# Kernel tuning notes

Measured on AMD Instinct MI355X. Metric: run time of the kernel, lower is better.

Reference implementation:

```python
import jax, jax.numpy as jnp
import numpy as np

CHANNELS = 768
N_HEADS = 12
HEAD_DIM = CHANNELS // N_HEADS
WINDOW = 4
B, T = 4, 1024


def setup_inputs() -> dict:
    key = jax.random.key(0)
    ks = jax.random.split(key, 11)
    C = CHANNELS
    s = 1.0 / np.sqrt(C)
    inp = {
        "x": jax.random.normal(ks[0], (B, C, T), dtype=jnp.float32),
        "w_q": jax.random.normal(ks[1], (C, C), dtype=jnp.float32) * s,
        "b_q": jnp.zeros((C,), dtype=jnp.float32),
        "w_k": jax.random.normal(ks[2], (C, C), dtype=jnp.float32) * s,
        "b_k": jnp.zeros((C,), dtype=jnp.float32),
        "w_v": jax.random.normal(ks[3], (C, C), dtype=jnp.float32) * s,
        "b_v": jnp.zeros((C,), dtype=jnp.float32),
        "w_o": jax.random.normal(ks[4], (C, C), dtype=jnp.float32) * s,
        "b_o": jnp.zeros((C,), dtype=jnp.float32),
        "emb_rel_k": jax.random.normal(ks[5], (2 * WINDOW + 1, HEAD_DIM), dtype=jnp.float32) * 0.01,
        "emb_rel_v": jax.random.normal(ks[6], (2 * WINDOW + 1, HEAD_DIM), dtype=jnp.float32) * 0.01,
    }
    return inp


def _rel_embeddings(emb_k, emb_v, t):
    pos = jnp.arange(t)
    rel_pos = pos[None, :] - pos[:, None]            # (T, T), rel_pos[i,j] = j - i
    outside = jnp.abs(rel_pos) > WINDOW
    rel_idx = jnp.clip(rel_pos, -WINDOW, WINDOW) + WINDOW
    rel_k = jnp.where(outside[:, :, None], 0.0, emb_k[rel_idx])  # (T, T, d)
    rel_v = jnp.where(outside[:, :, None], 0.0, emb_v[rel_idx])
    return rel_k, rel_v


def reference(x, w_q, b_q, w_k, b_k, w_v, b_v, w_o, b_o, emb_rel_k, emb_rel_v):
    Bq, C, t = x.shape
    H, d = N_HEADS, HEAD_DIM
    # 1x1 Conv1d == per-timestep linear over channels
    def proj(w, b):
        return jnp.einsum('oc,bct->bot', w, x) + b[None, :, None]
    # (B, C, T) -> (B, H, T, d)
    def split_heads(y):
        return y.reshape(Bq, H, d, t).transpose(0, 1, 3, 2)
    q = split_heads(proj(w_q, b_q)) / jnp.sqrt(jnp.float32(d))
    k = split_heads(proj(w_k, b_k))
    v = split_heads(proj(w_v, b_v))
    scores = jnp.einsum('bhid,bhjd->bhij', q, k)
    rel_k, rel_v = _rel_embeddings(emb_rel_k, emb_rel_v, t)
    scores = scores + jnp.einsum('bhid,ijd->bhij', q, rel_k)
    attn = jax.nn.softmax(scores, axis=-1)
    out = jnp.einsum('bhij,bhjd->bhid', attn, v)
    out = out + jnp.einsum('bhij,ijd->bhid', attn, rel_v)
    out = out.transpose(0, 1, 3, 2).reshape(Bq, C, t)  # (B, C, T)
    out = jnp.einsum('oc,bct->bot', w_o, out) + b_o[None, :, None]
    return out
```

## Files before the change

kernel.cpp:

```cpp
#include <hip/hip_runtime.h>

#define B_ 4
#define T_ 1024
#define C_ 768
#define H_ 12
#define D_ 64

typedef unsigned short u16;
typedef __attribute__((ext_vector_type(8))) short b16x8;
typedef __attribute__((ext_vector_type(4))) float f32x4;

#define MFMA(a, b, c) __builtin_amdgcn_mfma_f32_16x16x32_bf16(a, b, c, 0, 0, 0)

__device__ __forceinline__ float b2f(u16 u) {
    return __uint_as_float(((unsigned)u) << 16);
}
__device__ __forceinline__ u16 f2b(float f) {
    unsigned u = __float_as_uint(f);
    u += 0x7fffu + ((u >> 16) & 1u);
    return (u16)(u >> 16);
}

__device__ __forceinline__ void g2l16(const u16* g, u16* l) {
    __builtin_amdgcn_global_load_lds(
        (const __attribute__((address_space(1))) unsigned int*)g,
        (__attribute__((address_space(3))) unsigned int*)l, 16, 0, 0);
}

__global__ __launch_bounds__(256) void convw_kernel(
    const float* __restrict__ w0, const float* __restrict__ w1,
    const float* __restrict__ w2, const float* __restrict__ w3,
    u16* __restrict__ o)
{
    const float* src = blockIdx.y == 0 ? w0 : blockIdx.y == 1 ? w1 :
                       blockIdx.y == 2 ? w2 : w3;
    u16* dst = o + (size_t)blockIdx.y * C_ * C_;
    const int i = (blockIdx.x * 256 + threadIdx.x) * 4;
    float4 v = *(const float4*)(src + i);
    ushort4 st = {f2b(v.x), f2b(v.y), f2b(v.z), f2b(v.w)};
    *(ushort4*)(dst + i) = st;
}

__global__ __launch_bounds__(256) void convx_kernel(
    const float* __restrict__ x, u16* __restrict__ xb)
{
    __shared__ u16 tile[64][68];
    const int tid = threadIdx.x;
    const int t0 = blockIdx.x * 64, c0 = blockIdx.y * 64, b = blockIdx.z;
    #pragma unroll
    for (int p = 0; p < 4; ++p) {
        const int cc = p * 16 + (tid >> 4);
        const int t4 = (tid & 15) * 4;
        float4 v = *(const float4*)(x + ((size_t)b * C_ + c0 + cc) * T_ + t0 + t4);
        tile[t4 + 0][cc] = f2b(v.x);
        tile[t4 + 1][cc] = f2b(v.y);
        tile[t4 + 2][cc] = f2b(v.z);
        tile[t4 + 3][cc] = f2b(v.w);
    }
    __syncthreads();
    #pragma unroll
    for (int p = 0; p < 4; ++p) {
        const int tt = p * 16 + (tid >> 4);
        const int c4 = (tid & 15) * 4;
        ushort4 st = *(const ushort4*)&tile[tt][c4];
        *(ushort4*)(xb + ((size_t)b * T_ + t0 + tt) * C_ + c0 + c4) = st;
    }
}

__global__ __launch_bounds__(256) void qkv_mfma_kernel(
    const u16* __restrict__ wb, const u16* __restrict__ xb,
    const float* __restrict__ b_q, const float* __restrict__ b_k,
    const float* __restrict__ b_v,
    u16* __restrict__ q_ws, u16* __restrict__ k_ws, u16* __restrict__ v_ws)
{
    __shared__ u16 a_s[128 * 32];
    __shared__ u16 b_s[128 * 32];

    const int tid = threadIdx.x;
    const int wv = tid >> 6, lane = tid & 63;
    const int lo = lane & 15, quad = lane >> 4;
    const int wm = wv >> 1, wn = wv & 1;
    const int swz = (lo >> 1) & 3;
    const int srow = lane >> 2;
    const int skb  = (lane & 3) ^ ((lane >> 3) & 3);

    const int t0 = blockIdx.x * 128;
    const int mat = blockIdx.y / 6, oy = blockIdx.y % 6;
    const int o0 = oy * 128;
    const int b  = blockIdx.z;

    const u16* A = wb + (size_t)mat * C_ * C_;
    const float* bias = mat == 0 ? b_q : (mat == 1 ? b_k : b_v);
    u16* dst = mat == 0 ? q_ws : (mat == 1 ? k_ws : v_ws);
    const float scale = mat == 0 ? 0.125f : 1.0f;

    const size_t bT0 = (size_t)b * T_ + t0;

    f32x4 acc[4][4] = {};

    for (int kk = 0; kk < C_; kk += 32) {
        __syncthreads();
        #pragma unroll
        for (int ia = 0; ia < 2; ++ia) {
            const int row0 = (wv * 2 + ia) * 16;
            g2l16(A + (size_t)(o0 + row0 + srow) * C_ + kk + skb * 8,
                  a_s + row0 * 32);
        }
        #pragma unroll
        for (int ib = 0; ib < 2; ++ib) {
            const int row0 = (wv * 2 + ib) * 16;
            g2l16(xb + (bT0 + row0 + srow) * C_ + kk + skb * 8,
                  b_s + row0 * 32);
        }
        __syncthreads();

        b16x8 af[4], bf[4];
        #pragma unroll
        for (int mi = 0; mi < 4; ++mi) {
            const int m = wm * 64 + mi * 16 + lo;
            af[mi] = *(const b16x8*)(a_s + m * 32 + (quad ^ swz) * 8);
        }
        #pragma unroll
        for (int ni = 0; ni < 4; ++ni) {
            const int n = wn * 64 + ni * 16 + lo;
            bf[ni] = *(const b16x8*)(b_s + n * 32 + (quad ^ swz) * 8);
        }
        #pragma unroll
        for (int mi = 0; mi < 4; ++mi)
            #pragma unroll
            for (int ni = 0; ni < 4; ++ni)
                acc[mi][ni] = MFMA(af[mi], bf[ni], acc[mi][ni]);
    }

    #pragma unroll
    for (int mi = 0; mi < 4; ++mi) {
        const int o_b = o0 + wm * 64 + mi * 16 + quad * 4;
        const float4 bv4 = *(const float4*)(bias + o_b);
        const int h = o_b >> 6;
        const int dd0 = o_b & 63;
        #pragma unroll
        for (int ni = 0; ni < 4; ++ni) {
            const int t = t0 + wn * 64 + ni * 16 + lo;
            f32x4 a = acc[mi][ni];
            if (mat == 2) {
                v_ws[(((size_t)b * H_ + h) * D_ + dd0 + 0) * T_ + t] = f2b(a[0] + bv4.x);
                v_ws[(((size_t)b * H_ + h) * D_ + dd0 + 1) * T_ + t] = f2b(a[1] + bv4.y);
                v_ws[(((size_t)b * H_ + h) * D_ + dd0 + 2) * T_ + t] = f2b(a[2] + bv4.z);
                v_ws[(((size_t)b * H_ + h) * D_ + dd0 + 3) * T_ + t] = f2b(a[3] + bv4.w);
            } else {
                ushort4 st;
                st.x = f2b((a[0] + bv4.x) * scale);
                st.y = f2b((a[1] + bv4.y) * scale);
                st.z = f2b((a[2] + bv4.z) * scale);
                st.w = f2b((a[3] + bv4.w) * scale);
                *(ushort4*)(dst + (((size_t)b * H_ + h) * T_ + t) * D_ + dd0) = st;
            }
        }
    }
}

__global__ __launch_bounds__(256) void out_mfma_kernel(
    const u16* __restrict__ wob, const u16* __restrict__ ab,
    const float* __restrict__ bias, float* __restrict__ out)
{
    __shared__ u16 a_s[64 * 32];
    __shared__ u16 b_s[128 * 32];

    const int tid = threadIdx.x;
    const int wv = tid >> 6, lane = tid & 63;
    const int lo = lane & 15, quad = lane >> 4;
    const int wm = wv >> 1, wn = wv & 1;
    const int swz = (lo >> 1) & 3;
    const int srow = lane >> 2;
    const int skb  = (lane & 3) ^ ((lane >> 3) & 3);

    const int t0 = blockIdx.x * 128;
    const int o0 = blockIdx.y * 64;
    const int b  = blockIdx.z;
    const size_t bT0 = (size_t)b * T_ + t0;

    f32x4 acc[2][4] = {};

    for (int kk = 0; kk < C_; kk += 32) {
        __syncthreads();
        {
            const int row0 = wv * 16;
            g2l16(wob + (size_t)(o0 + row0 + srow) * C_ + kk + skb * 8,
                  a_s + row0 * 32);
        }
        #pragma unroll
        for (int ib = 0; ib < 2; ++ib) {
            const int row0 = (wv * 2 + ib) * 16;
            g2l16(ab + (bT0 + row0 + srow) * C_ + kk + skb * 8,
                  b_s + row0 * 32);
        }
        __syncthreads();

        b16x8 af[2], bf[4];
        #pragma unroll
        for (int mi = 0; mi < 2; ++mi) {
            const int m = wm * 32 + mi * 16 + lo;
            af[mi] = *(const b16x8*)(a_s + m * 32 + (quad ^ swz) * 8);
        }
        #pragma unroll
        for (int ni = 0; ni < 4; ++ni) {
            const int n = wn * 64 + ni * 16 + lo;
            bf[ni] = *(const b16x8*)(b_s + n * 32 + (quad ^ swz) * 8);
        }
        #pragma unroll
        for (int mi = 0; mi < 2; ++mi)
            #pragma unroll
            for (int ni = 0; ni < 4; ++ni)
                acc[mi][ni] = MFMA(af[mi], bf[ni], acc[mi][ni]);
    }

    #pragma unroll
    for (int mi = 0; mi < 2; ++mi) {
        const int o_b = o0 + wm * 32 + mi * 16 + quad * 4;
        const float4 bv4 = *(const float4*)(bias + o_b);
        const float bb[4] = {bv4.x, bv4.y, bv4.z, bv4.w};
        #pragma unroll
        for (int ni = 0; ni < 4; ++ni) {
            const int t = t0 + wn * 64 + ni * 16 + lo;
            f32x4 a = acc[mi][ni];
            #pragma unroll
            for (int r = 0; r < 4; ++r)
                out[((size_t)b * C_ + o_b + r) * T_ + t] = a[r] + bb[r];
        }
    }
}

__global__ __launch_bounds__(256, 2) void attn_mfma_kernel(
    const u16* __restrict__ qw, const u16* __restrict__ kw, const u16* __restrict__ vw,
    const float* __restrict__ erk, const float* __restrict__ erv,
    u16* __restrict__ att)
{
    __shared__ u16 k_s[64 * 72];
    __shared__ u16 v_s[64 * 72];
    __shared__ u16 p_s[128 * 72];
    __shared__ float qrel_s[128][9];
    __shared__ float band_s[128][9];
    __shared__ float alpha_s[128];

    const int tid = threadIdx.x;
    const int wv = tid >> 6, lane = tid & 63;
    const int lo = lane & 15, quad = lane >> 4;
    const int wi0 = wv * 32;
    const int it0 = blockIdx.x * 128;
    const int h = blockIdx.y, b = blockIdx.z;
    const int bh = b * H_ + h;

    const u16* qp = qw + (size_t)bh * T_ * D_;
    const u16* kp = kw + (size_t)bh * T_ * D_;
    const u16* vp = vw + (size_t)bh * D_ * T_;

    b16x8 qf[2][2];
    #pragma unroll
    for (int nt = 0; nt < 2; ++nt)
        #pragma unroll
        for (int kc = 0; kc < 2; ++kc)
            qf[nt][kc] = *(const b16x8*)(
                qp + (size_t)(it0 + wi0 + nt * 16 + lo) * D_ + kc * 32 + quad * 8);

    {
        b16x8 ekf[2];
        #pragma unroll
        for (int kc = 0; kc < 2; ++kc) {
            union { b16x8 v; u16 s[8]; } t;
            #pragma unroll
            for (int r = 0; r < 8; ++r) t.s[r] = 0;
            if (lo < 9) {
                const float* e = erk + lo * D_ + kc * 32 + quad * 8;
                #pragma unroll
                for (int r = 0; r < 8; ++r) t.s[r] = f2b(e[r]);
            }
            ekf[kc] = t.v;
        }
        #pragma unroll
        for (int it = 0; it < 2; ++it) {
            f32x4 acc = {};
            acc = MFMA(qf[it][0], ekf[0], acc);
            acc = MFMA(qf[it][1], ekf[1], acc);
            if (lo < 9)
                #pragma unroll
                for (int r = 0; r < 4; ++r)
                    qrel_s[wi0 + it * 16 + quad * 4 + r][lo] = acc[r];
        }
    }

    for (int idx = tid; idx < 128 * 9; idx += 256)
        (&band_s[0][0])[idx] = -1e30f;

    f32x4 o[2][4] = {};
    float mstate[2] = {-1e30f, -1e30f};
    float lstate[2] = {0.f, 0.f};

    for (int jt = 0; jt < T_; jt += 64) {
        __syncthreads();
        #pragma unroll
        for (int rnd = 0; rnd < 2; ++rnd) {
            const int c0 = tid + rnd * 256;
            const int row = c0 >> 3, ch = c0 & 7;
            *(b16x8*)(k_s + row * 72 + ch * 8) =
                *(const b16x8*)(kp + (size_t)(jt + row) * D_ + ch * 8);
            *(b16x8*)(v_s + row * 72 + ch * 8) =
                *(const b16x8*)(vp + (size_t)row * T_ + jt + ch * 8);
        }
        __syncthreads();

        f32x4 st[4][2];
        #pragma unroll
        for (int mt = 0; mt < 4; ++mt) {
            const b16x8 ka0 = *(const b16x8*)(k_s + (mt * 16 + lo) * 72 + quad * 8);
            const b16x8 ka1 = *(const b16x8*)(k_s + (mt * 16 + lo) * 72 + 32 + quad * 8);
            #pragma unroll
            for (int nt = 0; nt < 2; ++nt) {
                f32x4 a = {};
                a = MFMA(ka0, qf[nt][0], a);
                a = MFMA(ka1, qf[nt][1], a);
                st[mt][nt] = a;
            }
        }

        #pragma unroll
        for (int mt = 0; mt < 4; ++mt)
            #pragma unroll
            for (int nt = 0; nt < 2; ++nt)
                #pragma unroll
                for (int r = 0; r < 4; ++r) {
                    const int il = wi0 + nt * 16 + lo;
                    const int rr = (jt + mt * 16 + quad * 4 + r) - (it0 + il) + 4;
                    if (rr >= 0 && rr <= 8) {
                        const float s2 = st[mt][nt][r] + qrel_s[il][rr];
                        st[mt][nt][r] = s2;
                        band_s[il][rr] = s2;
                    }
                }

        #pragma unroll
        for (int nt = 0; nt < 2; ++nt) {
            float tm = -1e30f;
            #pragma unroll
            for (int mt = 0; mt < 4; ++mt)
                #pragma unroll
                for (int r = 0; r < 4; ++r)
                    tm = fmaxf(tm, st[mt][nt][r]);
            tm = fmaxf(tm, __shfl_xor(tm, 16));
            tm = fmaxf(tm, __shfl_xor(tm, 32));
            const float nm = fmaxf(mstate[nt], tm);
            const float al = __expf(mstate[nt] - nm);
            mstate[nt] = nm;
            float rs = 0.f;
            #pragma unroll
            for (int mt = 0; mt < 4; ++mt)
                #pragma unroll
                for (int r = 0; r < 4; ++r) {
                    const float e = __expf(st[mt][nt][r] - nm);
                    st[mt][nt][r] = e;
                    rs += e;
                }
            rs += __shfl_xor(rs, 16);
            rs += __shfl_xor(rs, 32);
            lstate[nt] = lstate[nt] * al + rs;
            if (quad == 0) alpha_s[wi0 + nt * 16 + lo] = al;
        }

        #pragma unroll
        for (int nt = 0; nt < 2; ++nt) {
            const int il = wi0 + nt * 16 + lo;
            #pragma unroll
            for (int mt = 0; mt < 4; ++mt) {
                ushort4 pw;
                pw.x = f2b(st[mt][nt][0]);
                pw.y = f2b(st[mt][nt][1]);
                pw.z = f2b(st[mt][nt][2]);
                pw.w = f2b(st[mt][nt][3]);
                *(ushort4*)(p_s + il * 72 + mt * 16 + quad * 4) = pw;
            }
        }

        #pragma unroll
        for (int it = 0; it < 2; ++it)
            #pragma unroll
            for (int r = 0; r < 4; ++r) {
                const float a = alpha_s[wi0 + it * 16 + quad * 4 + r];
                #pragma unroll
                for (int nd = 0; nd < 4; ++nd)
                    o[it][nd][r] *= a;
            }

        b16x8 vb[4][2];
        #pragma unroll
        for (int nd = 0; nd < 4; ++nd) {
            vb[nd][0] = *(const b16x8*)(v_s + (nd * 16 + lo) * 72 + quad * 8);
            vb[nd][1] = *(const b16x8*)(v_s + (nd * 16 + lo) * 72 + 32 + quad * 8);
        }
        #pragma unroll
        for (int it = 0; it < 2; ++it) {
            const b16x8 pa0 = *(const b16x8*)(p_s + (wi0 + it * 16 + lo) * 72 + quad * 8);
            const b16x8 pa1 = *(const b16x8*)(p_s + (wi0 + it * 16 + lo) * 72 + 32 + quad * 8);
            #pragma unroll
            for (int nd = 0; nd < 4; ++nd) {
                o[it][nd] = MFMA(pa0, vb[nd][0], o[it][nd]);
                o[it][nd] = MFMA(pa1, vb[nd][1], o[it][nd]);
            }
        }
    }

    b16x8 baf[2];
    #pragma unroll
    for (int it = 0; it < 2; ++it) {
        const int il = wi0 + it * 16 + lo;
        union { b16x8 v; u16 s[8]; } t;
        #pragma unroll
        for (int r = 0; r < 8; ++r) {
            const int rr = quad * 8 + r;
            const float e = (rr <= 8) ? __expf(band_s[il][rr] - mstate[it]) : 0.f;
            t.s[r] = f2b(e);
        }
        baf[it] = t.v;
    }
    #pragma unroll
    for (int nd = 0; nd < 4; ++nd) {
        union { b16x8 v; u16 s[8]; } t;
        #pragma unroll
        for (int r = 0; r < 8; ++r) {
            const int rr = quad * 8 + r;
            t.s[r] = (rr <= 8) ? f2b(erv[rr * D_ + nd * 16 + lo]) : (u16)0;
        }
        #pragma unroll
        for (int it = 0; it < 2; ++it)
            o[it][nd] = MFMA(baf[it], t.v, o[it][nd]);
    }

    #pragma unroll
    for (int nt = 0; nt < 2; ++nt)
        if (quad == 0) alpha_s[wi0 + nt * 16 + lo] = 1.f / lstate[nt];

    #pragma unroll
    for (int it = 0; it < 2; ++it)
        #pragma unroll
        for (int r = 0; r < 4; ++r) {
            const int il = wi0 + it * 16 + quad * 4 + r;
            const float li = alpha_s[il];
            const size_t base = ((size_t)b * T_ + it0 + il) * C_ + h * D_;
            #pragma unroll
            for (int nd = 0; nd < 4; ++nd)
                att[base + nd * 16 + lo] = f2b(o[it][nd][r] * li);
        }
}

extern "C" void kernel_launch(void* const* d_in, const int* in_sizes, int n_in,
                              void* d_out, int out_size, void* d_ws, size_t ws_size,
                              hipStream_t stream) {
    const float* x   = (const float*)d_in[0];
    const float* w_q = (const float*)d_in[1];
    const float* b_q = (const float*)d_in[2];
    const float* w_k = (const float*)d_in[3];
    const float* b_k = (const float*)d_in[4];
    const float* w_v = (const float*)d_in[5];
    const float* b_v = (const float*)d_in[6];
    const float* w_o = (const float*)d_in[7];
    const float* b_o = (const float*)d_in[8];
    const float* erk = (const float*)d_in[9];
    const float* erv = (const float*)d_in[10];

    const size_t N = (size_t)B_ * C_ * T_;
    u16* q_ws = (u16*)d_ws;
    u16* k_ws = q_ws + N;
    u16* v_ws = q_ws + 2 * N;
    u16* a_ws = q_ws + 3 * N;
    u16* xb   = q_ws + 4 * N;
    u16* wb   = q_ws + 5 * N;
    float* out = (float*)d_out;

    dim3 blk(256, 1, 1);

    convw_kernel<<<dim3(C_ * C_ / 1024, 4), blk, 0, stream>>>(w_q, w_k, w_v, w_o, wb);
    convx_kernel<<<dim3(T_ / 64, C_ / 64, B_), blk, 0, stream>>>(x, xb);

    qkv_mfma_kernel<<<dim3(T_ / 128, 18, B_), blk, 0, stream>>>(
        wb, xb, b_q, b_k, b_v, q_ws, k_ws, v_ws);

    attn_mfma_kernel<<<dim3(T_ / 128, H_, B_), blk, 0, stream>>>(
        q_ws, k_ws, v_ws, erk, erv, a_ws);

    out_mfma_kernel<<<dim3(T_ / 128, C_ / 64, B_), blk, 0, stream>>>(
        wb + 3 * (size_t)C_ * C_, a_ws, b_o, out);
}
```

Before: 194.6 us.

## Shrink attention query tile, add XOR-swizzled LDS via global_load_lds, separate V transpose

Result: faster. 174.6 us (-10.3%).

```diff
diff --git a/kernel.cpp b/kernel.cpp
--- a/kernel.cpp
+++ b/kernel.cpp
@@ -19,6 +19,9 @@
     unsigned u = __float_as_uint(f);
     u += 0x7fffu + ((u >> 16) & 1u);
     return (u16)(u >> 16);
+}
+__device__ __forceinline__ u16 f2b_tr(float f) {
+    return (u16)(__float_as_uint(f) >> 16);
 }
 
 __device__ __forceinline__ void g2l16(const u16* g, u16* l) {
@@ -73,8 +76,8 @@
     const float* __restrict__ b_v,
     u16* __restrict__ q_ws, u16* __restrict__ k_ws, u16* __restrict__ v_ws)
 {
-    __shared__ u16 a_s[128 * 32];
-    __shared__ u16 b_s[128 * 32];
+    __shared__ __align__(16) u16 a_s[128 * 32];
+    __shared__ __align__(16) u16 b_s[128 * 32];
 
     const int tid = threadIdx.x;
     const int wv = tid >> 6, lane = tid & 63;
@@ -142,20 +145,42 @@
         for (int ni = 0; ni < 4; ++ni) {
             const int t = t0 + wn * 64 + ni * 16 + lo;
             f32x4 a = acc[mi][ni];
-            if (mat == 2) {
-                v_ws[(((size_t)b * H_ + h) * D_ + dd0 + 0) * T_ + t] = f2b(a[0] + bv4.x);
-                v_ws[(((size_t)b * H_ + h) * D_ + dd0 + 1) * T_ + t] = f2b(a[1] + bv4.y);
-                v_ws[(((size_t)b * H_ + h) * D_ + dd0 + 2) * T_ + t] = f2b(a[2] + bv4.z);
-                v_ws[(((size_t)b * H_ + h) * D_ + dd0 + 3) * T_ + t] = f2b(a[3] + bv4.w);
-            } else {
-                ushort4 st;
-                st.x = f2b((a[0] + bv4.x) * scale);
-                st.y = f2b((a[1] + bv4.y) * scale);
-                st.z = f2b((a[2] + bv4.z) * scale);
-                st.w = f2b((a[3] + bv4.w) * scale);
-                *(ushort4*)(dst + (((size_t)b * H_ + h) * T_ + t) * D_ + dd0) = st;
-            }
-        }
+            ushort4 st;
+            st.x = f2b((a[0] + bv4.x) * scale);
+            st.y = f2b((a[1] + bv4.y) * scale);
+            st.z = f2b((a[2] + bv4.z) * scale);
+            st.w = f2b((a[3] + bv4.w) * scale);
+            *(ushort4*)(dst + (((size_t)b * H_ + h) * T_ + t) * D_ + dd0) = st;
+        }
+    }
+}
+
+__global__ __launch_bounds__(256) void transv_kernel(
+    const u16* __restrict__ src, u16* __restrict__ dst)
+{
+    __shared__ __align__(16) u16 tile[64 * 72];
+    const int tid = threadIdx.x;
+    const int t0 = blockIdx.x * 64;
+    const int bh = blockIdx.y;
+    const u16* s = src + (size_t)bh * T_ * D_;
+    u16* d = dst + (size_t)bh * D_ * T_;
+    #pragma unroll
+    for (int p = 0; p < 2; ++p) {
+        const int idx = tid + p * 256;
+        const int row = idx >> 3, ch = idx & 7;
+        *(b16x8*)(tile + row * 72 + ch * 8) =
+            *(const b16x8*)(s + (size_t)(t0 + row) * D_ + ch * 8);
+    }
+    __syncthreads();
+    #pragma unroll
+    for (int p = 0; p < 2; ++p) {
+        const int idx = tid + p * 256;
+        const int dd = idx >> 3, ch = idx & 7;
+        union { b16x8 v; u16 e[8]; } t;
+        #pragma unroll
+        for (int e = 0; e < 8; ++e)
+            t.e[e] = tile[(ch * 8 + e) * 72 + dd];
+        *(b16x8*)(d + (size_t)dd * T_ + t0 + ch * 8) = t.v;
     }
 }
 
@@ -163,8 +188,8 @@
     const u16* __restrict__ wob, const u16* __restrict__ ab,
     const float* __restrict__ bias, float* __restrict__ out)
 {
-    __shared__ u16 a_s[64 * 32];
-    __shared__ u16 b_s[128 * 32];
+    __shared__ __align__(16) u16 a_s[64 * 32];
+    __shared__ __align__(16) u16 b_s[128 * 32];
 
     const int tid = threadIdx.x;
     const int wv = tid >> 6, lane = tid & 63;
@@ -235,18 +260,18 @@
     const float* __restrict__ erk, const float* __restrict__ erv,
     u16* __restrict__ att)
 {
-    __shared__ u16 k_s[64 * 72];
-    __shared__ u16 v_s[64 * 72];
-    __shared__ u16 p_s[128 * 72];
-    __shared__ float qrel_s[128][9];
-    __shared__ float band_s[128][9];
-    __shared__ float alpha_s[128];
+    __shared__ __align__(16) u16 k_s[64 * 64];
+    __shared__ __align__(16) u16 v_s[64 * 64];
+    __shared__ __align__(16) u16 p_s[64 * 64];
+    __shared__ float qrel_s[64][9];
+    __shared__ float band_s[64][9];
+    __shared__ float alpha_s[64];
 
     const int tid = threadIdx.x;
     const int wv = tid >> 6, lane = tid & 63;
     const int lo = lane & 15, quad = lane >> 4;
-    const int wi0 = wv * 32;
-    const int it0 = blockIdx.x * 128;
+    const int wi0 = wv * 16;
+    const int it0 = blockIdx.x * 64;
     const int h = blockIdx.y, b = blockIdx.z;
     const int bh = b * H_ + h;
 
@@ -254,13 +279,14 @@
     const u16* kp = kw + (size_t)bh * T_ * D_;
     const u16* vp = vw + (size_t)bh * D_ * T_;
 
-    b16x8 qf[2][2];
-    #pragma unroll
-    for (int nt = 0; nt < 2; ++nt)
-        #pragma unroll
-        for (int kc = 0; kc < 2; ++kc)
-            qf[nt][kc] = *(const b16x8*)(
-                qp + (size_t)(it0 + wi0 + nt * 16 + lo) * D_ + kc * 32 + quad * 8);
+    const int srow = lane >> 3;
+    const int schunk = (lane & 7) ^ (srow & 7);
+    const int lsw = lo & 7;
+
+    b16x8 qf[2];
+    #pragma unroll
+    for (int kc = 0; kc < 2; ++kc)
+        qf[kc] = *(const b16x8*)(qp + (size_t)(it0 + wi0 + lo) * D_ + kc * 32 + quad * 8);
 
     {
         b16x8 ekf[2];
@@ -276,178 +302,142 @@
             }
             ekf[kc] = t.v;
         }
-        #pragma unroll
-        for (int it = 0; it < 2; ++it) {
-            f32x4 acc = {};
-            acc = MFMA(qf[it][0], ekf[0], acc);
-            acc = MFMA(qf[it][1], ekf[1], acc);
-            if (lo < 9)
-                #pragma unroll
-                for (int r = 0; r < 4; ++r)
-                    qrel_s[wi0 + it * 16 + quad * 4 + r][lo] = acc[r];
-        }
-    }
-
-    for (int idx = tid; idx < 128 * 9; idx += 256)
-        (&band_s[0][0])[idx] = -1e30f;
-
-    f32x4 o[2][4] = {};
-    float mstate[2] = {-1e30f, -1e30f};
-    float lstate[2] = {0.f, 0.f};
+        f32x4 acc = {};
+        acc = MFMA(qf[0], ekf[0], acc);
+        acc = MFMA(qf[1], ekf[1], acc);
+        if (lo < 9)
+            #pragma unroll
+            for (int r = 0; r < 4; ++r)
+                qrel_s[wi0 + quad * 4 + r][lo] = acc[r];
+    }
+
+    for (int idx = lane; idx < 16 * 9; idx += 64)
+        band_s[wi0 + idx / 9][idx % 9] = -1e30f;
+
+    f32x4 o[4] = {};
+    float m = -1e30f, l = 0.f;
 
     for (int jt = 0; jt < T_; jt += 64) {
         __syncthreads();
         #pragma unroll
-        for (int rnd = 0; rnd < 2; ++rnd) {
-            const int c0 = tid + rnd * 256;
-            const int row = c0 >> 3, ch = c0 & 7;
-            *(b16x8*)(k_s + row * 72 + ch * 8) =
-                *(const b16x8*)(kp + (size_t)(jt + row) * D_ + ch * 8);
-            *(b16x8*)(v_s + row * 72 + ch * 8) =
-                *(const b16x8*)(vp + (size_t)row * T_ + jt + ch * 8);
-        }
-        __syncthreads();
-
-        f32x4 st[4][2];
+        for (int i2 = 0; i2 < 2; ++i2) {
+            const int row0 = (wv * 2 + i2) * 8;
+            g2l16(kp + (size_t)(jt + row0 + srow) * D_ + schunk * 8, k_s + row0 * 64);
+            g2l16(vp + (size_t)(row0 + srow) * T_ + jt + schunk * 8, v_s + row0 * 64);
+        }
+        __syncthreads();
+
+        f32x4 st[4];
         #pragma unroll
         for (int mt = 0; mt < 4; ++mt) {
-            const b16x8 ka0 = *(const b16x8*)(k_s + (mt * 16 + lo) * 72 + quad * 8);
-            const b16x8 ka1 = *(const b16x8*)(k_s + (mt * 16 + lo) * 72 + 32 + quad * 8);
-            #pragma unroll
-            for (int nt = 0; nt < 2; ++nt) {
-                f32x4 a = {};
-                a = MFMA(ka0, qf[nt][0], a);
-                a = MFMA(ka1, qf[nt][1], a);
-                st[mt][nt] = a;
+            const int kr = mt * 16 + lo;
+            const b16x8 ka0 = *(const b16x8*)(k_s + kr * 64 + ((quad) ^ lsw) * 8);
+            const b16x8 ka1 = *(const b16x8*)(k_s + kr * 64 + ((4 + quad) ^ lsw) * 8);
+            f32x4 a = {};
+            a = MFMA(ka0, qf[0], a);
+            a = MFMA(ka1, qf[1], a);
+            st[mt] = a;
+        }
+
+        const int ibase = it0 + wi0 + lo;
+        #pragma unroll
+        for (int mt = 0; mt < 4; ++mt)
+            #pragma unroll
+            for (int r = 0; r < 4; ++r) {
+                const int rr = (jt + mt * 16 + quad * 4 + r) - ibase + 4;
+                if (rr >= 0 && rr <= 8) {
+                    const float s2 = st[mt][r] + qrel_s[wi0 + lo][rr];
+                    st[mt][r] = s2;
+                    band_s[wi0 + lo][rr] = s2;
+                }
             }
-        }
-
+
+        float tm = -1e30f;
         #pragma unroll
         for (int mt = 0; mt < 4; ++mt)
             #pragma unroll
-            for (int nt = 0; nt < 2; ++nt)
-                #pragma unroll
-                for (int r = 0; r < 4; ++r) {
-                    const int il = wi0 + nt * 16 + lo;
-                    const int rr = (jt + mt * 16 + quad * 4 + r) - (it0 + il) + 4;
-                    if (rr >= 0 && rr <= 8) {
-                        const float s2 = st[mt][nt][r] + qrel_s[il][rr];
-                        st[mt][nt][r] = s2;
-                        band_s[il][rr] = s2;
-                    }
-                }
-
-        #pragma unroll
-        for (int nt = 0; nt < 2; ++nt) {
-            float tm = -1e30f;
-            #pragma unroll
-            for (int mt = 0; mt < 4; ++mt)
-                #pragma unroll
-                for (int r = 0; r < 4; ++r)
-                    tm = fmaxf(tm, st[mt][nt][r]);
-            tm = fmaxf(tm, __shfl_xor(tm, 16));
-            tm = fmaxf(tm, __shfl_xor(tm, 32));
-            const float nm = fmaxf(mstate[nt], tm);
-            const float al = __expf(mstate[nt] - nm);
-            mstate[nt] = nm;
-            float rs = 0.f;
-            #pragma unroll
-            for (int mt = 0; mt < 4; ++mt)
-                #pragma unroll
-                for (int r = 0; r < 4; ++r) {
-                    const float e = __expf(st[mt][nt][r] - nm);
-                    st[mt][nt][r] = e;
-                    rs += e;
-                }
-            rs += __shfl_xor(rs, 16);
-            rs += __shfl_xor(rs, 32);
-            lstate[nt] = lstate[nt] * al + rs;
-            if (quad == 0) alpha_s[wi0 + nt * 16 + lo] = al;
-        }
-
-        #pragma unroll
-        for (int nt = 0; nt < 2; ++nt) {
-            const int il = wi0 + nt * 16 + lo;
-            #pragma unroll
-            for (int mt = 0; mt < 4; ++mt) {
-                ushort4 pw;
-                pw.x = f2b(st[mt][nt][0]);
-                pw.y = f2b(st[mt][nt][1]);
-                pw.z = f2b(st[mt][nt][2]);
-                pw.w = f2b(st[mt][nt][3]);
-                *(ushort4*)(p_s + il * 72 + mt * 16 + quad * 4) = pw;
+            for (int r = 0; r < 4; ++r)
+                tm = fmaxf(tm, st[mt][r]);
+        tm = fmaxf(tm, __shfl_xor(tm, 16));
+        tm = fmaxf(tm, __shfl_xor(tm, 32));
+        const float nm = fmaxf(m, tm);
+        const float al = __expf(m - nm);
+        m = nm;
+        float rs = 0.f;
+        #pragma unroll
+        for (int mt = 0; mt < 4; ++mt)
+            #pragma unroll
+            for (int r = 0; r < 4; ++r) {
+                const float e = __expf(st[mt][r] - nm);
+                st[mt][r] = e;
+                rs += e;
             }
-        }
-
-        #pragma unroll
-        for (int it = 0; it < 2; ++it)
-            #pragma unroll
-            for (int r = 0; r < 4; ++r) {
-                const float a = alpha_s[wi0 + it * 16 + quad * 4 + r];
-                #pragma unroll
-                for (int nd = 0; nd < 4; ++nd)
-                    o[it][nd][r] *= a;
-            }
-
-        b16x8 vb[4][2];
+        rs += __shfl_xor(rs, 16);
+        rs += __shfl_xor(rs, 32);
+        l = l * al + rs;
+        if (quad == 0) alpha_s[wi0 + lo] = al;
+
+        #pragma unroll
+        for (int mt = 0; mt < 4; ++mt) {
+            ushort4 pw;
+            pw.x = f2b_tr(st[mt][0]);
+            pw.y = f2b_tr(st[mt][1]);
+            pw.z = f2b_tr(st[mt][2]);
+            pw.w = f2b_tr(st[mt][3]);
+            const int slot = (mt * 2 + (quad >> 1)) ^ lsw;
+            *(ushort4*)(p_s + (wi0 + lo) * 64 + slot * 8 + (quad & 1) * 4) = pw;
+        }
+
+        #pragma unroll
+        for (int r = 0; r < 4; ++r) {
+            const float a = alpha_s[wi0 + quad * 4 + r];
+            #pragma unroll
+            for (int nd = 0; nd < 4; ++nd)
+                o[nd][r] *= a;
+        }
+
+        const b16x8 pa0 = *(const b16x8*)(p_s + (wi0 + lo) * 64 + ((quad) ^ lsw) * 8);
+        const b16x8 pa1 = *(const b16x8*)(p_s + (wi0 + lo) * 64 + ((4 + quad) ^ lsw) * 8);
         #pragma unroll
         for (int nd = 0; nd < 4; ++nd) {
-            vb[nd][0] = *(const b16x8*)(v_s + (nd * 16 + lo) * 72 + quad * 8);
-            vb[nd][1] = *(const b16x8*)(v_s + (nd * 16 + lo) * 72 + 32 + quad * 8);
-        }
-        #pragma unroll
-        for (int it = 0; it < 2; ++it) {
-            const b16x8 pa0 = *(const b16x8*)(p_s + (wi0 + it * 16 + lo) * 72 + quad * 8);
-            const b16x8 pa1 = *(const b16x8*)(p_s + (wi0 + it * 16 + lo) * 72 + 32 + quad * 8);
-            #pragma unroll
-            for (int nd = 0; nd < 4; ++nd) {
-                o[it][nd] = MFMA(pa0, vb[nd][0], o[it][nd]);
-                o[it][nd] = MFMA(pa1, vb[nd][1], o[it][nd]);
-            }
-        }
-    }
-
-    b16x8 baf[2];
-    #pragma unroll
-    for (int it = 0; it < 2; ++it) {
-        const int il = wi0 + it * 16 + lo;
-        union { b16x8 v; u16 s[8]; } t;
+            const int vr = nd * 16 + lo;
+            const b16x8 vb0 = *(const b16x8*)(v_s + vr * 64 + ((quad) ^ lsw) * 8);
+            const b16x8 vb1 = *(const b16x8*)(v_s + vr * 64 + ((4 + quad) ^ lsw) * 8);
+            o[nd] = MFMA(pa0, vb0, o[nd]);
+            o[nd] = MFMA(pa1, vb1, o[nd]);
+        }
+    }
+
+    {
+        union { b16x8 v; u16 s[8]; } tb;
         #pragma unroll
         for (int r = 0; r < 8; ++r) {
             const int rr = quad * 8 + r;
-            const float e = (rr <= 8) ? __expf(band_s[il][rr] - mstate[it]) : 0.f;
-            t.s[r] = f2b(e);
-        }
-        baf[it] = t.v;
-    }
-    #pragma unroll
-    for (int nd = 0; nd < 4; ++nd) {
-        union { b16x8 v; u16 s[8]; } t;
-        #pragma unroll
-        for (int r = 0; r < 8; ++r) {
-            const int rr = quad * 8 + r;
-            t.s[r] = (rr <= 8) ? f2b(erv[rr * D_ + nd * 16 + lo]) : (u16)0;
-        }
-        #pragma unroll
-        for (int it = 0; it < 2; ++it)
-            o[it][nd] = MFMA(baf[it], t.v, o[it][nd]);
-    }
-
-    #pragma unroll
-    for (int nt = 0; nt < 2; ++nt)
-        if (quad == 0) alpha_s[wi0 + nt * 16 + lo] = 1.f / lstate[nt];
-
-    #pragma unroll
-    for (int it = 0; it < 2; ++it)
-        #pragma unroll
-        for (int r = 0; r < 4; ++r) {
-            const int il = wi0 + it * 16 + quad * 4 + r;
-            const float li = alpha_s[il];
-            const size_t base = ((size_t)b * T_ + it0 + il) * C_ + h * D_;
-            #pragma unroll
-            for (int nd = 0; nd < 4; ++nd)
-                att[base + nd * 16 + lo] = f2b(o[it][nd][r] * li);
-        }
+            tb.s[r] = (rr <= 8) ? f2b(__expf(band_s[wi0 + lo][rr] - m)) : (u16)0;
+        }
+        const b16x8 baf = tb.v;
+        #pragma unroll
+        for (int nd = 0; nd < 4; ++nd) {
+            union { b16x8 v; u16 s[8]; } t;
+            #pragma unroll
+            for (int r = 0; r < 8; ++r) {
+                const int rr = quad * 8 + r;
+                t.s[r] = (rr <= 8) ? f2b(erv[rr * D_ + nd * 16 + lo]) : (u16)0;
+            }
+            o[nd] = MFMA(baf, t.v, o[nd]);
+        }
+    }
+
+    if (quad == 0) alpha_s[wi0 + lo] = 1.f / l;
+    #pragma unroll
+    for (int r = 0; r < 4; ++r) {
+        const int il = wi0 + quad * 4 + r;
+        const float inv = alpha_s[il];
+        const size_t base = ((size_t)b * T_ + it0 + il) * C_ + h * D_;
+        #pragma unroll
+        for (int nd = 0; nd < 4; ++nd)
+            att[base + nd * 16 + lo] = f2b(o[nd][r] * inv);
+    }
 }
 
 extern "C" void kernel_launch(void* const* d_in, const int* in_sizes, int n_in,
@@ -466,12 +456,13 @@
     const float* erv = (const float*)d_in[10];
 
     const size_t N = (size_t)B_ * C_ * T_;
-    u16* q_ws = (u16*)d_ws;
-    u16* k_ws = q_ws + N;
-    u16* v_ws = q_ws + 2 * N;
-    u16* a_ws = q_ws + 3 * N;
-    u16* xb   = q_ws + 4 * N;
-    u16* wb   = q_ws + 5 * N;
+    u16* q_ws  = (u16*)d_ws;
+    u16* k_ws  = q_ws + N;
+    u16* vraw  = q_ws + 2 * N;
+    u16* vdT   = q_ws + 3 * N;
+    u16* xb    = q_ws + 4 * N;
+    u16* a_ws  = vraw;
+    u16* wb    = q_ws + 5 * N;
     float* out = (float*)d_out;
 
     dim3 blk(256, 1, 1);
@@ -480,10 +471,12 @@
     convx_kernel<<<dim3(T_ / 64, C_ / 64, B_), blk, 0, stream>>>(x, xb);
 
     qkv_mfma_kernel<<<dim3(T_ / 128, 18, B_), blk, 0, stream>>>(
-        wb, xb, b_q, b_k, b_v, q_ws, k_ws, v_ws);
-
-    attn_mfma_kernel<<<dim3(T_ / 128, H_, B_), blk, 0, stream>>>(
-        q_ws, k_ws, v_ws, erk, erv, a_ws);
+        wb, xb, b_q, b_k, b_v, q_ws, k_ws, vraw);
+
+    transv_kernel<<<dim3(T_ / 64, H_ * B_), blk, 0, stream>>>(vraw, vdT);
+
+    attn_mfma_kernel<<<dim3(T_ / 64, H_, B_), blk, 0, stream>>>(
+        q_ws, k_ws, vdT, erk, erv, a_ws);
 
     out_mfma_kernel<<<dim3(T_ / 128, C_ / 64, B_), blk, 0, stream>>>(
         wb + 3 * (size_t)C_ * C_, a_ws, b_o, out);
```
